# Optimization experiments

Hardware: AMD Instinct MI355X
Metric: run time of the kernel (lower is better)

## Reference

```python
import jax, jax.numpy as jnp
import numpy as np

L, N, E, H, D, F = 2048, 2, 1024, 16, 64, 4096  # seq, batch, embed, heads, head_dim, ffn
EPS = 1e-5


def _ln(x, w, b):
    m = jnp.mean(x, axis=-1, keepdims=True)
    v = jnp.mean(jnp.square(x - m), axis=-1, keepdims=True)
    return (x - m) * jax.lax.rsqrt(v + EPS) * w + b


def setup_inputs() -> dict:
    key = jax.random.key(0)
    ks = jax.random.split(key, 16)
    s = 0.02
    f32 = jnp.float32
    return {
        "x": jax.random.normal(ks[0], (L, N, E), f32),
        "ln1_w": jnp.ones((E,), f32),
        "ln1_b": jnp.zeros((E,), f32),
        "wq": jax.random.normal(ks[1], (H * D, E), f32) * s,
        "bq": jnp.zeros((H * D,), f32),
        "wk": jax.random.normal(ks[2], (H * D, E), f32) * s,
        "bk": jnp.zeros((H * D,), f32),
        "wv": jax.random.normal(ks[3], (H * D, E), f32) * s,
        "bv": jnp.zeros((H * D,), f32),
        "wout": jax.random.normal(ks[4], (E, H * D), f32) * s,
        "bout": jnp.zeros((E,), f32),
        "ln2_w": jnp.ones((E,), f32),
        "ln2_b": jnp.zeros((E,), f32),
        "fc1_w": jax.random.normal(ks[5], (F, E), f32) * s,
        "fc1_b": jnp.zeros((F,), f32),
        "fc2_w": jax.random.normal(ks[6], (E, F), f32) * s,
        "fc2_b": jnp.zeros((E,), f32),
    }


def reference(x, ln1_w, ln1_b, wq, bq, wk, bk, wv, bv, wout, bout,
              ln2_w, ln2_b, fc1_w, fc1_b, fc2_w, fc2_b):
    scale = D ** (-0.5)
    residual = x
    h = _ln(x, ln1_w, ln1_b)                      # (L,N,E)
    q = (h @ wq.T + bq).reshape(L, N, H, D) * scale
    k = (h @ wk.T + bk).reshape(L, N, H, D)
    v = (h @ wv.T + bv).reshape(L, N, H, D)
    attn = jnp.einsum('qnhd,knhd->nhqk', q, k)    # (N,H,L,L) full score matrix
    causal = jnp.tril(jnp.ones((L, L), bool))
    attn = jnp.where(causal[None, None], attn, jnp.float32(-10000.0))
    p = jax.nn.softmax(attn, axis=-1)
    o = jnp.einsum('nhqk,knhd->qnhd', p, v).reshape(L, N, H * D)
    o = o @ wout.T + bout
    x = o + residual
    residual = x
    h = _ln(x, ln2_w, ln2_b)
    h = jax.nn.gelu(h @ fc1_w.T + fc1_b, approximate=False)
    h = h @ fc2_w.T + fc2_b
    return h + residual
```

## Files before the change

### kernel.cpp

```cpp
#include <hip/hip_runtime.h>
#include <hip/hip_bf16.h>
#include <math.h>

using bf16 = __hip_bfloat16;
typedef __bf16 bf16x8 __attribute__((ext_vector_type(8)));
typedef short  short4v __attribute__((ext_vector_type(4)));
typedef float  f32x4  __attribute__((ext_vector_type(4)));

static constexpr int Lq = 2048, Nb = 2, E = 1024, Hh = 16, Dd = 64, Ff = 4096;
static constexpr int MT = Lq * Nb;
static constexpr int QKLD = 2 * E;
static constexpr int LDL = 2 * QKLD;

__device__ __forceinline__ void async_lds16(const void* g, void* l) {
  __builtin_amdgcn_global_load_lds(
      (const __attribute__((address_space(1))) void*)g,
      (__attribute__((address_space(3))) void*)l, 16, 0, 0);
}
__device__ __forceinline__ bf16x8 ld8(const bf16* p) { return *(const bf16x8*)p; }
__device__ __forceinline__ short bfbits(float x) {
  bf16 t = __float2bfloat16(x);
  return *(short*)&t;
}
__device__ __forceinline__ float gelu_fast(float v) {
  const float y = fminf(2.302208f * (v + 0.044715f * v * v * v), 80.f);
  const float t = exp2f(y);
  return v * t / (t + 1.0f);
}

__global__ __launch_bounds__(256) void cvt_all_kernel(
    const float* __restrict__ wq, const float* __restrict__ wk,
    const float* __restrict__ wv, const float* __restrict__ wout,
    const float* __restrict__ fc1w, const float* __restrict__ fc2w,
    bf16* __restrict__ wqkvb, bf16* __restrict__ woutb,
    bf16* __restrict__ f1wb, bf16* __restrict__ f2wb) {
  const int i = blockIdx.x * 256 + threadIdx.x;
  const float* src;
  bf16* dst;
  size_t off;
  if (i < 786432) {
    const int r = i >> 18;
    off = (size_t)(i & 262143);
    src = (r == 0) ? wq : (r == 1) ? wk : wv;
    dst = wqkvb + (size_t)r * (E * E);
  } else if (i < 1048576) {
    off = (size_t)(i - 786432); src = wout; dst = woutb;
  } else if (i < 2097152) {
    off = (size_t)(i - 1048576); src = fc1w; dst = f1wb;
  } else {
    off = (size_t)(i - 2097152); src = fc2w; dst = f2wb;
  }
  float4 v = ((const float4*)src)[off];
  bf16 o4[4] = {__float2bfloat16(v.x), __float2bfloat16(v.y),
                __float2bfloat16(v.z), __float2bfloat16(v.w)};
  *(uint2*)(dst + 4 * off) = *(uint2*)o4;
}

template <int EPI, int BK>
__global__ __launch_bounds__(256) void gemm_bt(
    const bf16* __restrict__ A, const bf16* __restrict__ W,
    const float* __restrict__ b1, const float* __restrict__ b2,
    const float* __restrict__ b3, int Klen, int Kstride, int Nld,
    float qscale, int scut, bf16* __restrict__ outb,
    bf16* __restrict__ outv) {
  __shared__ __align__(16) bf16 As[128 * BK];
  __shared__ __align__(16) bf16 Bs[128 * BK];
  const int tid = threadIdx.x;
  const int w = tid >> 6, lane = tid & 63;
  const int quad = lane >> 4, l16 = lane & 15;
  const int wm = (w >> 1) * 64, wn = (w & 1) * 64;
  const int m0 = blockIdx.y * 128, n0 = blockIdx.x * 128;
  const int koff = blockIdx.z * Klen;

  f32x4 acc[4][4];
#pragma unroll
  for (int i = 0; i < 4; i++)
#pragma unroll
    for (int j = 0; j < 4; j++)
#pragma unroll
      for (int r = 0; r < 4; r++) acc[i][j][r] = 0.f;

  if constexpr (BK == 32) {
    const int c0 = w * 64 + lane;
    const int c1 = c0 + 256;
    const size_t arow0 = (size_t)(m0 + (c0 >> 2)), arow1 = (size_t)(m0 + (c1 >> 2));
    const size_t brow0 = (size_t)(n0 + (c0 >> 2)), brow1 = (size_t)(n0 + (c1 >> 2));
    const int col0 = (c0 & 3) * 8, col1 = (c1 & 3) * 8;
    bf16* ldsA0 = &As[(w * 64) * 8];
    bf16* ldsA1 = &As[(256 + w * 64) * 8];
    bf16* ldsB0 = &Bs[(w * 64) * 8];
    bf16* ldsB1 = &Bs[(256 + w * 64) * 8];

    const int nk = Klen >> 5;
    for (int kt = 0; kt < nk; ++kt) {
      const int k0 = koff + kt * 32;
      async_lds16(A + arow0 * Kstride + k0 + col0, ldsA0);
      async_lds16(A + arow1 * Kstride + k0 + col1, ldsA1);
      async_lds16(W + brow0 * Kstride + k0 + col0, ldsB0);
      async_lds16(W + brow1 * Kstride + k0 + col1, ldsB1);
      __syncthreads();
      bf16x8 a[4], b[4];
#pragma unroll
      for (int i = 0; i < 4; i++) {
        a[i] = ld8(&As[(wm + i * 16 + l16) * 32 + quad * 8]);
        b[i] = ld8(&Bs[(wn + i * 16 + l16) * 32 + quad * 8]);
      }
#pragma unroll
      for (int i = 0; i < 4; i++)
#pragma unroll
        for (int j = 0; j < 4; j++)
          acc[i][j] = __builtin_amdgcn_mfma_f32_16x16x32_bf16(a[i], b[j], acc[i][j], 0, 0, 0);
      __syncthreads();
    }
  } else {
    const int rowoff = w * 8 + (lane >> 3);
    const int colsw = (((lane & 7) ^ (lane >> 3)) << 3);

    const int nk = Klen >> 6;
    for (int kt = 0; kt < nk; ++kt) {
      const int k0 = koff + (kt << 6);
#pragma unroll
      for (int r = 0; r < 4; r++) {
        async_lds16(A + (size_t)(m0 + r * 32 + rowoff) * Kstride + k0 + colsw,
                    As + (size_t)(r * 256 + w * 64) * 8);
        async_lds16(W + (size_t)(n0 + r * 32 + rowoff) * Kstride + k0 + colsw,
                    Bs + (size_t)(r * 256 + w * 64) * 8);
      }
      __syncthreads();
#pragma unroll
      for (int ksub = 0; ksub < 2; ksub++) {
        const int gx = ksub * 4 + quad;
        bf16x8 a[4], b[4];
#pragma unroll
        for (int i = 0; i < 4; i++) {
          const int ra = wm + i * 16 + l16;
          const int rb = wn + i * 16 + l16;
          a[i] = ld8(&As[(size_t)(ra * 8 + (gx ^ (l16 & 7))) * 8]);
          b[i] = ld8(&Bs[(size_t)(rb * 8 + (gx ^ (l16 & 7))) * 8]);
        }
#pragma unroll
        for (int i = 0; i < 4; i++)
#pragma unroll
          for (int j = 0; j < 4; j++)
            acc[i][j] = __builtin_amdgcn_mfma_f32_16x16x32_bf16(a[i], b[j], acc[i][j], 0, 0, 0);
      }
      __syncthreads();
    }
  }

  const size_t zoff = (EPI == 3) ? (size_t)blockIdx.z * ((size_t)MT * E) : 0;
#pragma unroll
  for (int i = 0; i < 4; i++) {
    const int mrow = m0 + wm + i * 16 + quad * 4;
#pragma unroll
    for (int j = 0; j < 4; j++) {
      const int ncol = n0 + wn + j * 16 + l16;
      float bv = 0.f;
      if constexpr (EPI != 3) {
        if (b3 != nullptr) {
          bv = (ncol < 1024) ? b1[ncol]
               : (ncol < 2048) ? b2[ncol - 1024] : b3[ncol - 2048];
        } else {
          bv = b1[ncol];
        }
      }
      const float sc = (ncol < scut) ? qscale : 1.0f;
#pragma unroll
      for (int r = 0; r < 4; r++) {
        float v = (acc[i][j][r] + bv) * sc;
        if constexpr (EPI == 2) {
          outb[(size_t)(mrow + r) * Nld + ncol] = __float2bfloat16(gelu_fast(v));
        } else if constexpr (EPI == 3) {
          outb[zoff + (size_t)(mrow + r) * Nld + ncol] = __float2bfloat16(v);
        } else {
          if (ncol < 2048) {
            outb[(size_t)(mrow + r) * 2048 + ncol] = __float2bfloat16(v);
          } else {
            const int h = (ncol - 2048) >> 6, d = ncol & 63;
            const int tok = mrow + r, n = tok & 1, l = tok >> 1;
            outv[(size_t)((n * 16 + h) * 64 + d) * Lq + l] = __float2bfloat16(v);
          }
        }
      }
    }
  }
}

template <int S, int H>
__device__ __forceinline__ void load_frags256(const char* Ab, const char* Bb,
                                              const int (&aoff)[8], const int (&boff)[4],
                                              bf16x8 (&a)[4], bf16x8 (&b)[4]) {
#pragma unroll
  for (int i = 0; i < 4; i++) a[i] = ld8((const bf16*)(Ab + S * 16384 + aoff[H * 4 + i]));
#pragma unroll
  for (int j = 0; j < 4; j++) b[j] = ld8((const bf16*)(Bb + S * 16384 + boff[j]));
}

template <int H>
__device__ __forceinline__ void mfma256(const bf16x8 (&a)[4], const bf16x8 (&b)[4],
                                        f32x4 (&acc)[8][4]) {
#pragma unroll
  for (int i = 0; i < 4; i++)
#pragma unroll
    for (int j = 0; j < 4; j++)
      acc[H * 4 + i][j] =
          __builtin_amdgcn_mfma_f32_16x16x32_bf16(a[i], b[j], acc[H * 4 + i][j], 0, 0, 0);
}

template <int K, int NOUT>
__global__ __launch_bounds__(512, 2) void gemm256_gelu(
    const bf16* __restrict__ A, const bf16* __restrict__ W,
    const float* __restrict__ bias, bf16* __restrict__ out) {
  extern __shared__ char smem[];
  constexpr int NKT = K / 64;
  static_assert(NKT >= 2, "need >=2 K-tiles");
  const int tid = threadIdx.x;
  const int w = tid >> 6, lane = tid & 63;
  const int quad = lane >> 4, l16 = lane & 15;
  const int wr = w >> 2, wc = w & 3;
  const int m0 = blockIdx.y * 256, n0 = blockIdx.x * 256;

  const int o0 = tid << 4;
  const int o1 = o0 + 8192;
  const int r0 = o0 >> 6, r1 = o1 >> 6;
  const int c0 = ((((o0 >> 4) & 3) ^ ((o0 >> 7) & 3)) << 3);
  const int c1 = ((((o1 >> 4) & 3) ^ ((o1 >> 7) & 3)) << 3);
  const bf16* Ag0 = A + (size_t)(m0 + r0) * K + c0;
  const bf16* Ag1 = A + (size_t)(m0 + r1) * K + c1;
  const bf16* Wg0 = W + (size_t)(n0 + r0) * K + c0;
  const bf16* Wg1 = W + (size_t)(n0 + r1) * K + c1;
  const int ldsw = w << 10;

  int aoff[8], boff[4];
#pragma unroll
  for (int h = 0; h < 2; h++)
#pragma unroll
    for (int i = 0; i < 4; i++) {
      const int ra = wr * 128 + h * 64 + i * 16 + l16;
      aoff[h * 4 + i] = ra * 64 + ((quad ^ ((ra >> 1) & 3)) << 4);
    }
#pragma unroll
  for (int j = 0; j < 4; j++) {
    const int rb = wc * 64 + j * 16 + l16;
    boff[j] = rb * 64 + ((quad ^ ((rb >> 1) & 3)) << 4);
  }

  f32x4 acc[8][4];
#pragma unroll
  for (int i = 0; i < 8; i++)
#pragma unroll
    for (int j = 0; j < 4; j++)
#pragma unroll
      for (int r = 0; r < 4; r++) acc[i][j][r] = 0.f;

  {
    char* d = smem;
    async_lds16(Ag0, d + ldsw);
    async_lds16(Ag1, d + 8192 + ldsw);
    async_lds16(Wg0, d + 32768 + ldsw);
    async_lds16(Wg1, d + 32768 + 8192 + ldsw);
    async_lds16(Ag0 + 32, d + 16384 + ldsw);
    async_lds16(Ag1 + 32, d + 16384 + 8192 + ldsw);
    async_lds16(Wg0 + 32, d + 49152 + ldsw);
    async_lds16(Wg1 + 32, d + 49152 + 8192 + ldsw);
  }
  asm volatile("s_waitcnt vmcnt(4)" ::: "memory");
  __builtin_amdgcn_s_barrier();

  for (int kt = 0; kt < NKT; ++kt) {
    const char* Ab = smem + ((kt & 1) << 16);
    const char* Bb = Ab + 32768;
    char* Sd = smem + (((kt + 1) & 1) << 16);
    const int kn = (kt + 1) << 6;
    if (kt + 1 < NKT) {
      {
        bf16x8 a[4], b[4];
        load_frags256<0, 0>(Ab, Bb, aoff, boff, a, b);
        async_lds16(Ag0 + kn, Sd + ldsw);
        async_lds16(Ag1 + kn, Sd + 8192 + ldsw);
        __builtin_amdgcn_s_barrier();
        __builtin_amdgcn_s_setprio(1);
        mfma256<0>(a, b, acc);
        __builtin_amdgcn_s_setprio(0);
        __builtin_amdgcn_sched_barrier(0);
        __builtin_amdgcn_s_barrier();
      }
      {
        bf16x8 a[4], b[4];
        load_frags256<0, 1>(Ab, Bb, aoff, boff, a, b);
        async_lds16(Wg0 + kn, Sd + 32768 + ldsw);
        async_lds16(Wg1 + kn, Sd + 32768 + 8192 + ldsw);
        __builtin_amdgcn_s_barrier();
        __builtin_amdgcn_s_setprio(1);
        mfma256<1>(a, b, acc);
        __builtin_amdgcn_s_setprio(0);
        asm volatile("s_waitcnt vmcnt(4)" ::: "memory");
        __builtin_amdgcn_sched_barrier(0);
        __builtin_amdgcn_s_barrier();
      }
      {
        bf16x8 a[4], b[4];
        load_frags256<1, 0>(Ab, Bb, aoff, boff, a, b);
        async_lds16(Ag0 + kn + 32, Sd + 16384 + ldsw);
        async_lds16(Ag1 + kn + 32, Sd + 16384 + 8192 + ldsw);
        __builtin_amdgcn_s_barrier();
        __builtin_amdgcn_s_setprio(1);
        mfma256<0>(a, b, acc);
        __builtin_amdgcn_s_setprio(0);
        __builtin_amdgcn_sched_barrier(0);
        __builtin_amdgcn_s_barrier();
      }
      {
        bf16x8 a[4], b[4];
        load_frags256<1, 1>(Ab, Bb, aoff, boff, a, b);
        async_lds16(Wg0 + kn + 32, Sd + 49152 + ldsw);
        async_lds16(Wg1 + kn + 32, Sd + 49152 + 8192 + ldsw);
        __builtin_amdgcn_s_barrier();
        __builtin_amdgcn_s_setprio(1);
        mfma256<1>(a, b, acc);
        __builtin_amdgcn_s_setprio(0);
        asm volatile("s_waitcnt vmcnt(4)" ::: "memory");
        __builtin_amdgcn_sched_barrier(0);
        __builtin_amdgcn_s_barrier();
      }
    } else {
      {
        bf16x8 a[4], b[4];
        load_frags256<0, 0>(Ab, Bb, aoff, boff, a, b);
        __builtin_amdgcn_s_barrier();
        __builtin_amdgcn_s_setprio(1);
        mfma256<0>(a, b, acc);
        __builtin_amdgcn_s_setprio(0);
        __builtin_amdgcn_sched_barrier(0);
        __builtin_amdgcn_s_barrier();
      }
      {
        bf16x8 a[4], b[4];
        load_frags256<0, 1>(Ab, Bb, aoff, boff, a, b);
        __builtin_amdgcn_s_barrier();
        __builtin_amdgcn_s_setprio(1);
        mfma256<1>(a, b, acc);
        __builtin_amdgcn_s_setprio(0);
        asm volatile("s_waitcnt vmcnt(0)" ::: "memory");
        __builtin_amdgcn_sched_barrier(0);
        __builtin_amdgcn_s_barrier();
      }
      {
        bf16x8 a[4], b[4];
        load_frags256<1, 0>(Ab, Bb, aoff, boff, a, b);
        __builtin_amdgcn_s_barrier();
        __builtin_amdgcn_s_setprio(1);
        mfma256<0>(a, b, acc);
        __builtin_amdgcn_s_setprio(0);
        __builtin_amdgcn_sched_barrier(0);
        __builtin_amdgcn_s_barrier();
      }
      {
        bf16x8 a[4], b[4];
        load_frags256<1, 1>(Ab, Bb, aoff, boff, a, b);
        __builtin_amdgcn_s_barrier();
        __builtin_amdgcn_s_setprio(1);
        mfma256<1>(a, b, acc);
        __builtin_amdgcn_s_setprio(0);
      }
    }
  }

#pragma unroll
  for (int j = 0; j < 4; j++) {
    const int col = n0 + wc * 64 + j * 16 + l16;
    const float bv = bias[col];
#pragma unroll
    for (int mI = 0; mI < 8; mI++) {
      const int row = m0 + wr * 128 + mI * 16 + quad * 4;
#pragma unroll
      for (int r = 0; r < 4; r++) {
        out[(size_t)(row + r) * NOUT + col] =
            __float2bfloat16(gelu_fast(acc[mI][j][r] + bv));
      }
    }
  }
}

__global__ __launch_bounds__(256) void reduce2_kernel(
    const bf16* __restrict__ P, const float* __restrict__ bias,
    const float* __restrict__ res, float* __restrict__ out) {
  const int i = blockIdx.x * 256 + threadIdx.x;
  const size_t e0 = (size_t)i * 4;
  const int col = (int)(e0 & (E - 1));
  uint2 u0 = *(const uint2*)(P + e0);
  uint2 u1 = *(const uint2*)(P + (size_t)MT * E + e0);
  const bf16* p0 = (const bf16*)&u0;
  const bf16* p1 = (const bf16*)&u1;
  float4 b = *(const float4*)(bias + col);
  float4 r = *(const float4*)(res + e0);
  float4 o;
  o.x = (float)p0[0] + (float)p1[0] + b.x + r.x;
  o.y = (float)p0[1] + (float)p1[1] + b.y + r.y;
  o.z = (float)p0[2] + (float)p1[2] + b.z + r.z;
  o.w = (float)p0[3] + (float)p1[3] + b.w + r.w;
  *(float4*)(out + e0) = o;
}

__global__ __launch_bounds__(256) void redln_kernel(
    const bf16* __restrict__ P, const float* __restrict__ bias,
    const float* __restrict__ res, const float* __restrict__ wgt,
    const float* __restrict__ bia, float* __restrict__ x1,
    bf16* __restrict__ h2) {
  const int t = blockIdx.x, tid = threadIdx.x;
  const size_t base = (size_t)t * E;
  const int e0 = tid * 4;
  uint2 u0 = *(const uint2*)(P + base + e0);
  uint2 u1 = *(const uint2*)(P + (size_t)MT * E + base + e0);
  const bf16* p0 = (const bf16*)&u0;
  const bf16* p1 = (const bf16*)&u1;
  float4 b = *(const float4*)(bias + e0);
  float4 r = *(const float4*)(res + base + e0);
  float v4[4];
  v4[0] = (float)p0[0] + (float)p1[0] + b.x + r.x;
  v4[1] = (float)p0[1] + (float)p1[1] + b.y + r.y;
  v4[2] = (float)p0[2] + (float)p1[2] + b.z + r.z;
  v4[3] = (float)p0[3] + (float)p1[3] + b.w + r.w;
  *(float4*)(x1 + base + e0) = *(float4*)v4;

  float s = 0.f, ss = 0.f;
#pragma unroll
  for (int i = 0; i < 4; i++) { s += v4[i]; ss += v4[i] * v4[i]; }
  for (int off = 32; off > 0; off >>= 1) {
    s += __shfl_down(s, off, 64);
    ss += __shfl_down(ss, off, 64);
  }
  __shared__ float rs[4], rss[4], mv[2];
  const int w = tid >> 6;
  if ((tid & 63) == 0) { rs[w] = s; rss[w] = ss; }
  __syncthreads();
  if (tid == 0) {
    float S = rs[0] + rs[1] + rs[2] + rs[3];
    float SS = rss[0] + rss[1] + rss[2] + rss[3];
    float mean = S * (1.f / E);
    float var = SS * (1.f / E) - mean * mean;
    mv[0] = mean; mv[1] = rsqrtf(var + 1e-5f);
  }
  __syncthreads();
  const float mean = mv[0], rstd = mv[1];
  float4 wg = *(const float4*)(wgt + e0);
  float4 bb = *(const float4*)(bia + e0);
  bf16 o4[4];
  o4[0] = __float2bfloat16((v4[0] - mean) * rstd * wg.x + bb.x);
  o4[1] = __float2bfloat16((v4[1] - mean) * rstd * wg.y + bb.y);
  o4[2] = __float2bfloat16((v4[2] - mean) * rstd * wg.z + bb.z);
  o4[3] = __float2bfloat16((v4[3] - mean) * rstd * wg.w + bb.w);
  *(uint2*)(h2 + base + e0) = *(uint2*)o4;
}

__global__ __launch_bounds__(256) void ln_kernel(
    const float* __restrict__ x, const float* __restrict__ wgt,
    const float* __restrict__ bia, bf16* __restrict__ out) {
  const int t = blockIdx.x, tid = threadIdx.x;
  const size_t base = (size_t)t * E;
  float v4[4], s = 0.f, ss = 0.f;
#pragma unroll
  for (int i = 0; i < 4; i++) {
    float v = x[base + i * 256 + tid];
    v4[i] = v; s += v; ss += v * v;
  }
  for (int off = 32; off > 0; off >>= 1) {
    s += __shfl_down(s, off, 64);
    ss += __shfl_down(ss, off, 64);
  }
  __shared__ float rs[4], rss[4], mv[2];
  const int w = tid >> 6;
  if ((tid & 63) == 0) { rs[w] = s; rss[w] = ss; }
  __syncthreads();
  if (tid == 0) {
    float S = rs[0] + rs[1] + rs[2] + rs[3];
    float SS = rss[0] + rss[1] + rss[2] + rss[3];
    float mean = S * (1.f / E);
    float var = SS * (1.f / E) - mean * mean;
    mv[0] = mean; mv[1] = rsqrtf(var + 1e-5f);
  }
  __syncthreads();
  const float mean = mv[0], rstd = mv[1];
#pragma unroll
  for (int i = 0; i < 4; i++) {
    const int e = i * 256 + tid;
    float r = (v4[i] - mean) * rstd * wgt[e] + bia[e];
    out[base + e] = __float2bfloat16(r);
  }
}

__global__ __launch_bounds__(256) void attn_kernel(
    const bf16* __restrict__ QK, const bf16* __restrict__ VT,
    bf16* __restrict__ O) {
  __shared__ __align__(16) bf16 KB[512 * 8];
  __shared__ __align__(16) bf16 VB[512 * 8];
  const int tid = threadIdx.x;
  const int w = tid >> 6, lane = tid & 63, quad = lane >> 4, l16 = lane & 15;
  const int bid = blockIdx.x;
  const int x = bid & 7;
  const int m = (bid >> 3) & 31;
  const int g = bid >> 8;
  const int j = m >> 2;
  const int hh = (m & 3) * 8 + x;
  const int qt = (g == 0) ? j : (g == 1) ? (31 - j) : (g == 2) ? (j + 8) : (23 - j);
  const int n = hh >> 4, h = hh & 15;

  const bf16* Qp = QK + n * QKLD + h * Dd;
  const bf16* Kp = Qp + E;
  const bf16* Vp = VT + (size_t)hh * 64 * Lq;

  bf16* ldsK0 = KB + (size_t)(w * 64) * 8;
  bf16* ldsK1 = KB + (size_t)(256 + w * 64) * 8;
  bf16* ldsV0 = VB + (size_t)(w * 64) * 8;
  bf16* ldsV1 = VB + (size_t)(256 + w * 64) * 8;
  const int w8 = w * 8;

  const int ql = qt * 64 + w * 16 + l16;
  const bf16x8 aq0 = ld8(Qp + (size_t)ql * LDL + quad * 8);
  const bf16x8 aq1 = ld8(Qp + (size_t)ql * LDL + 32 + quad * 8);

  f32x4 o_acc[4];
#pragma unroll
  for (int d = 0; d < 4; d++)
#pragma unroll
    for (int r = 0; r < 4; r++) o_acc[d][r] = 0.f;
  float m_run = -3e30f, l_run = 0.f;

  for (int kt = 0; kt <= qt; ++kt) {
    const size_t kb = (size_t)kt * 64;

    async_lds16(Kp + (size_t)(kb + lane) * LDL + w8, ldsK0);
    async_lds16(Kp + (size_t)(kb + lane) * LDL + 32 + w8, ldsK1);
    async_lds16(Vp + (size_t)lane * Lq + kb + w8, ldsV0);
    async_lds16(Vp + (size_t)lane * Lq + kb + 32 + w8, ldsV1);
    __syncthreads();

    f32x4 s[4];
#pragma unroll
    for (int ks = 0; ks < 4; ks++) {
      const bf16x8 kc0 = ld8(&KB[(size_t)((quad)*64 + ks * 16 + l16) * 8]);
      const bf16x8 kc1 = ld8(&KB[(size_t)((4 + quad) * 64 + ks * 16 + l16) * 8]);
#pragma unroll
      for (int r = 0; r < 4; r++) s[ks][r] = 0.f;
      s[ks] = __builtin_amdgcn_mfma_f32_16x16x32_bf16(kc0, aq0, s[ks], 0, 0, 0);
      s[ks] = __builtin_amdgcn_mfma_f32_16x16x32_bf16(kc1, aq1, s[ks], 0, 0, 0);
    }

    if (kt == qt) {
#pragma unroll
      for (int ks = 0; ks < 4; ks++) {
#pragma unroll
        for (int r = 0; r < 4; r++) {
          const int kg = kt * 64 + ks * 16 + quad * 4 + r;
          if (kg > ql) s[ks][r] = -14427.0f;
        }
      }
    }

    float tmax = s[0][0];
#pragma unroll
    for (int ks = 0; ks < 4; ks++)
#pragma unroll
      for (int r = 0; r < 4; r++) tmax = fmaxf(tmax, s[ks][r]);
    tmax = fmaxf(tmax, __shfl_xor(tmax, 16, 64));
    tmax = fmaxf(tmax, __shfl_xor(tmax, 32, 64));
    const float mnew = fmaxf(m_run, tmax);
    const float alpha = exp2f(m_run - mnew);
    m_run = mnew;
    float rsum = 0.f;
    short4v pf[4];
#pragma unroll
    for (int ks = 0; ks < 4; ks++) {
#pragma unroll
      for (int r = 0; r < 4; r++) {
        const float pv = exp2f(s[ks][r] - mnew);
        rsum += pv;
        pf[ks][r] = bfbits(pv);
      }
    }
    rsum += __shfl_xor(rsum, 16, 64);
    rsum += __shfl_xor(rsum, 32, 64);
    l_run = l_run * alpha + rsum;
#pragma unroll
    for (int d = 0; d < 4; d++)
#pragma unroll
      for (int r = 0; r < 4; r++) o_acc[d][r] *= alpha;

#pragma unroll
    for (int d = 0; d < 4; d++) {
#pragma unroll
      for (int ks = 0; ks < 4; ks++) {
        const int gg = ks * 2 + (quad >> 1);
        const short4v av =
            *(const short4v*)&VB[(size_t)(gg * 64 + d * 16 + l16) * 8 + (quad & 1) * 4];
        o_acc[d] = __builtin_amdgcn_mfma_f32_16x16x16bf16_1k(av, pf[ks], o_acc[d], 0, 0, 0);
      }
    }
    __syncthreads();
  }

  const float inv_l = 1.f / fmaxf(l_run, 1e-30f);
  const size_t obase = (size_t)ql * (Nb * E) + (size_t)n * E + h * Dd;
#pragma unroll
  for (int d = 0; d < 4; d++)
#pragma unroll
    for (int r = 0; r < 4; r++)
      O[obase + d * 16 + quad * 4 + r] = __float2bfloat16(o_acc[d][r] * inv_l);
}

extern "C" void kernel_launch(void* const* d_in, const int* in_sizes, int n_in,
                              void* d_out, int out_size, void* d_ws, size_t ws_size,
                              hipStream_t stream) {
  const float* x    = (const float*)d_in[0];
  const float* ln1w = (const float*)d_in[1];
  const float* ln1b = (const float*)d_in[2];
  const float* wq   = (const float*)d_in[3];
  const float* bq   = (const float*)d_in[4];
  const float* wk   = (const float*)d_in[5];
  const float* bk   = (const float*)d_in[6];
  const float* wv   = (const float*)d_in[7];
  const float* bv   = (const float*)d_in[8];
  const float* wout = (const float*)d_in[9];
  const float* bout = (const float*)d_in[10];
  const float* ln2w = (const float*)d_in[11];
  const float* ln2b = (const float*)d_in[12];
  const float* fc1w = (const float*)d_in[13];
  const float* fc1b = (const float*)d_in[14];
  const float* fc2w = (const float*)d_in[15];
  const float* fc2b = (const float*)d_in[16];

  char* ws = (char*)d_ws;
  bf16* wqkvb = (bf16*)(ws);
  bf16* woutb = (bf16*)(ws + ((size_t)6 << 20));
  bf16* f1wb  = (bf16*)(ws + ((size_t)8 << 20));
  bf16* f2wb  = (bf16*)(ws + ((size_t)16 << 20));
  bf16* h1    = (bf16*)(ws + ((size_t)24 << 20));
  bf16* qk    = (bf16*)(ws + ((size_t)32 << 20));
  bf16* vtg   = (bf16*)(ws + ((size_t)48 << 20));
  bf16* o     = (bf16*)(ws + ((size_t)56 << 20));
  float* x1   = (float*)(ws + ((size_t)64 << 20));
  bf16* Pout  = (bf16*)(ws + ((size_t)32 << 20));
  bf16* P01   = (bf16*)(ws);
  bf16* f1    = (bf16*)(ws + ((size_t)32 << 20));
  bf16* h2    = h1;
  float* outp = (float*)d_out;

  static bool g_shmem_attr = false;
  if (!g_shmem_attr) {
    hipFuncSetAttribute(reinterpret_cast<const void*>(gemm256_gelu<1024, 4096>),
                        hipFuncAttributeMaxDynamicSharedMemorySize, 131072);
    g_shmem_attr = true;
  }

  cvt_all_kernel<<<12288, 256, 0, stream>>>(wq, wk, wv, wout, fc1w, fc2w,
                                            wqkvb, woutb, f1wb, f2wb);

  ln_kernel<<<MT, 256, 0, stream>>>(x, ln1w, ln1b, h1);

  dim3 gQKV(3 * E / 128, MT / 128);
  dim3 gE2(E / 128, MT / 128, 2);

  gemm_bt<4, 64><<<gQKV, 256, 0, stream>>>(h1, wqkvb, bq, bk, bv, E, E, 2048,
                                           0.125f * 1.44269504f, 1024, qk, vtg);

  attn_kernel<<<1024, 256, 0, stream>>>(qk, vtg, o);

  gemm_bt<3, 64><<<gE2, 256, 0, stream>>>(o, woutb, nullptr, nullptr, nullptr,
                                          E / 2, E, E, 1.f, 0, Pout, nullptr);
  redln_kernel<<<MT, 256, 0, stream>>>(Pout, bout, x, ln2w, ln2b, x1, h2);

  gemm256_gelu<1024, 4096><<<dim3(Ff / 256, MT / 256), 512, 131072, stream>>>(
      h2, f1wb, fc1b, f1);

  gemm_bt<3, 64><<<gE2, 256, 0, stream>>>(f1, f2wb, nullptr, nullptr, nullptr,
                                          Ff / 2, Ff, E, 1.f, 0, P01, nullptr);
  reduce2_kernel<<<MT * E / 1024, 256, 0, stream>>>(P01, fc2b, x1, outp);
}
```

Baseline: 375.5 us.

## Double-buffer attention K/V tiles, add lazy softmax rescale and MFMA priority

The attention kernel now keeps two LDS buffers for K and V. It prefetches the next key tile with async global-to-LDS loads while the current tile is being computed, and waits with explicit vmcnt counts instead of full syncthreads. The online softmax skips the max update and accumulator rescale unless some lane's tile max exceeds the running max by more than 8 (log2 domain), which removes most rescale multiplies. MFMA sections are also wrapped in s_setprio. The costs are double the LDS footprint, and the raw waitcnt and barrier sequencing is fragile because it depends on how the compiler orders memory operations.

```diff
diff --git a/kernel.cpp b/kernel.cpp
--- a/kernel.cpp
+++ b/kernel.cpp
@@ -492,8 +492,8 @@
 __global__ __launch_bounds__(256) void attn_kernel(
     const bf16* __restrict__ QK, const bf16* __restrict__ VT,
     bf16* __restrict__ O) {
-  __shared__ __align__(16) bf16 KB[512 * 8];
-  __shared__ __align__(16) bf16 VB[512 * 8];
+  __shared__ __align__(16) bf16 KB[2][512 * 8];
+  __shared__ __align__(16) bf16 VB[2][512 * 8];
   const int tid = threadIdx.x;
   const int w = tid >> 6, lane = tid & 63, quad = lane >> 4, l16 = lane & 15;
   const int bid = blockIdx.x;
@@ -508,16 +508,17 @@
   const bf16* Qp = QK + n * QKLD + h * Dd;
   const bf16* Kp = Qp + E;
   const bf16* Vp = VT + (size_t)hh * 64 * Lq;
-
-  bf16* ldsK0 = KB + (size_t)(w * 64) * 8;
-  bf16* ldsK1 = KB + (size_t)(256 + w * 64) * 8;
-  bf16* ldsV0 = VB + (size_t)(w * 64) * 8;
-  bf16* ldsV1 = VB + (size_t)(256 + w * 64) * 8;
   const int w8 = w * 8;
 
   const int ql = qt * 64 + w * 16 + l16;
   const bf16x8 aq0 = ld8(Qp + (size_t)ql * LDL + quad * 8);
   const bf16x8 aq1 = ld8(Qp + (size_t)ql * LDL + 32 + quad * 8);
+  asm volatile("s_waitcnt vmcnt(0)" ::: "memory");
+
+  async_lds16(Kp + (size_t)lane * LDL + w8, &KB[0][(size_t)(w * 64) * 8]);
+  async_lds16(Kp + (size_t)lane * LDL + 32 + w8, &KB[0][(size_t)(256 + w * 64) * 8]);
+  async_lds16(Vp + (size_t)lane * Lq + w8, &VB[0][(size_t)(w * 64) * 8]);
+  async_lds16(Vp + (size_t)lane * Lq + 32 + w8, &VB[0][(size_t)(256 + w * 64) * 8]);
 
   f32x4 o_acc[4];
 #pragma unroll
@@ -527,24 +528,36 @@
   float m_run = -3e30f, l_run = 0.f;
 
   for (int kt = 0; kt <= qt; ++kt) {
-    const size_t kb = (size_t)kt * 64;
-
-    async_lds16(Kp + (size_t)(kb + lane) * LDL + w8, ldsK0);
-    async_lds16(Kp + (size_t)(kb + lane) * LDL + 32 + w8, ldsK1);
-    async_lds16(Vp + (size_t)lane * Lq + kb + w8, ldsV0);
-    async_lds16(Vp + (size_t)lane * Lq + kb + 32 + w8, ldsV1);
-    __syncthreads();
+    const bf16* KBb = KB[kt & 1];
+    const bf16* VBb = VB[kt & 1];
+    if (kt < qt) {
+      const size_t kb2 = (size_t)(kt + 1) * 64;
+      bf16* Kd = &KB[(kt & 1) ^ 1][0];
+      bf16* Vd = &VB[(kt & 1) ^ 1][0];
+      async_lds16(Kp + (size_t)(kb2 + lane) * LDL + w8, Kd + (size_t)(w * 64) * 8);
+      async_lds16(Kp + (size_t)(kb2 + lane) * LDL + 32 + w8,
+                  Kd + (size_t)(256 + w * 64) * 8);
+      async_lds16(Vp + (size_t)lane * Lq + kb2 + w8, Vd + (size_t)(w * 64) * 8);
+      async_lds16(Vp + (size_t)lane * Lq + kb2 + 32 + w8,
+                  Vd + (size_t)(256 + w * 64) * 8);
+      asm volatile("s_waitcnt vmcnt(4)" ::: "memory");
+    } else {
+      asm volatile("s_waitcnt vmcnt(0)" ::: "memory");
+    }
+    __builtin_amdgcn_s_barrier();
 
     f32x4 s[4];
+    __builtin_amdgcn_s_setprio(1);
 #pragma unroll
     for (int ks = 0; ks < 4; ks++) {
-      const bf16x8 kc0 = ld8(&KB[(size_t)((quad)*64 + ks * 16 + l16) * 8]);
-      const bf16x8 kc1 = ld8(&KB[(size_t)((4 + quad) * 64 + ks * 16 + l16) * 8]);
+      const bf16x8 kc0 = ld8(&KBb[(size_t)((quad)*64 + ks * 16 + l16) * 8]);
+      const bf16x8 kc1 = ld8(&KBb[(size_t)((4 + quad) * 64 + ks * 16 + l16) * 8]);
 #pragma unroll
       for (int r = 0; r < 4; r++) s[ks][r] = 0.f;
       s[ks] = __builtin_amdgcn_mfma_f32_16x16x32_bf16(kc0, aq0, s[ks], 0, 0, 0);
       s[ks] = __builtin_amdgcn_mfma_f32_16x16x32_bf16(kc1, aq1, s[ks], 0, 0, 0);
     }
+    __builtin_amdgcn_s_setprio(0);
 
     if (kt == qt) {
 #pragma unroll
@@ -564,39 +577,48 @@
       for (int r = 0; r < 4; r++) tmax = fmaxf(tmax, s[ks][r]);
     tmax = fmaxf(tmax, __shfl_xor(tmax, 16, 64));
     tmax = fmaxf(tmax, __shfl_xor(tmax, 32, 64));
-    const float mnew = fmaxf(m_run, tmax);
-    const float alpha = exp2f(m_run - mnew);
-    m_run = mnew;
+    float mbase = m_run;
+    if (__any(tmax - m_run > 8.0f)) {
+      const float mnew = fmaxf(m_run, tmax);
+      const float alpha = exp2f(m_run - mnew);
+      m_run = mnew;
+      mbase = mnew;
+      l_run *= alpha;
+#pragma unroll
+      for (int d = 0; d < 4; d++)
+#pragma unroll
+        for (int r = 0; r < 4; r++) o_acc[d][r] *= alpha;
+    }
     float rsum = 0.f;
     short4v pf[4];
 #pragma unroll
     for (int ks = 0; ks < 4; ks++) {
 #pragma unroll
       for (int r = 0; r < 4; r++) {
-        const float pv = exp2f(s[ks][r] - mnew);
+        const float pv = exp2f(s[ks][r] - mbase);
         rsum += pv;
         pf[ks][r] = bfbits(pv);
       }
     }
     rsum += __shfl_xor(rsum, 16, 64);
     rsum += __shfl_xor(rsum, 32, 64);
-    l_run = l_run * alpha + rsum;
-#pragma unroll
-    for (int d = 0; d < 4; d++)
-#pragma unroll
-      for (int r = 0; r < 4; r++) o_acc[d][r] *= alpha;
-
+    l_run += rsum;
+
+    __builtin_amdgcn_s_setprio(1);
 #pragma unroll
     for (int d = 0; d < 4; d++) {
 #pragma unroll
       for (int ks = 0; ks < 4; ks++) {
         const int gg = ks * 2 + (quad >> 1);
         const short4v av =
-            *(const short4v*)&VB[(size_t)(gg * 64 + d * 16 + l16) * 8 + (quad & 1) * 4];
+            *(const short4v*)&VBb[(size_t)(gg * 64 + d * 16 + l16) * 8 + (quad & 1) * 4];
         o_acc[d] = __builtin_amdgcn_mfma_f32_16x16x16bf16_1k(av, pf[ks], o_acc[d], 0, 0, 0);
       }
     }
-    __syncthreads();
+    __builtin_amdgcn_s_setprio(0);
+
+    __builtin_amdgcn_sched_barrier(0);
+    __builtin_amdgcn_s_barrier();
   }
 
   const float inv_l = 1.f / fmaxf(l_run, 1e-30f);
```

New measurement: 368.9 us. About the same (-1.8%).
